# Kernel tuning notes

Measured on AMD Instinct MI355X. Metric: run time of the kernel, lower is better.

## Reference

```python
import jax, jax.numpy as jnp
import numpy as np

B, D, T = 4, 1024, 512      # z: [B, input_dim, T]
V, CD = 32000, 4096          # codebook: [codebook_size, codebook_dim]
EPS = 1e-12                  # F.normalize default eps


def setup_inputs() -> dict:
    key = jax.random.key(0)
    k1, k2, k3, k4 = jax.random.split(key, 4)
    z = jax.random.normal(k1, (B, D, T), dtype=jnp.float32)
    codebook = jax.random.normal(k2, (V, CD), dtype=jnp.float32) * 0.02
    cb_w = jax.random.normal(k3, (D, CD), dtype=jnp.float32) * 0.02  # torch Linear weight [out,in]
    cb_b = jax.random.normal(k4, (D,), dtype=jnp.float32) * 0.02
    return {"z": z, "codebook": codebook, "cb_w": cb_w, "cb_b": cb_b}


def _l2norm(x):
    n = jnp.sqrt(jnp.sum(x * x, axis=1, keepdims=True))
    return x / jnp.maximum(n, EPS)


def reference(z, codebook, cb_w, cb_b):
    # stride == 1, use_cblinear == True -> z_e = z
    z_e = z                                              # [B, D, T]
    proj_cb = codebook @ cb_w.T + cb_b                    # [V, D] cb_proj(codebook)

    # decode_latents
    enc = jnp.transpose(z_e, (0, 2, 1)).reshape(-1, D)    # (B*T, D)
    enc_n = _l2norm(enc)
    cb_n = _l2norm(proj_cb)
    dist = (jnp.sum(enc_n * enc_n, axis=1, keepdims=True)
            - 2.0 * enc_n @ cb_n.T
            + jnp.sum(cb_n * cb_n, axis=1)[None, :])      # (B*T, V)
    indices = jnp.argmax(-dist, axis=1).reshape(B, T)     # argmin distance
    z_q = jnp.transpose(proj_cb[indices], (0, 2, 1))      # gather un-normalized codes -> [B, D, T]

    commitment_loss = jnp.mean((z_e - jax.lax.stop_gradient(z_q)) ** 2, axis=(1, 2))  # [B]
    codebook_loss = jnp.mean((z_q - jax.lax.stop_gradient(z_e)) ** 2, axis=(1, 2))    # [B]
    z_q_st = z_e + jax.lax.stop_gradient(z_q - z_e)       # straight-through
    return z_q_st, indices, commitment_loss, codebook_loss
```

## Files before the change

### kernel.cpp

```cpp
#include <hip/hip_runtime.h>
#include <hip/hip_bf16.h>
#include <math.h>

#define B_  4
#define D_  1024
#define T_  512
#define V_  32000
#define CD_ 4096
#define NR  (B_*T_)
#define VT2 (V_/256)

typedef __attribute__((ext_vector_type(8))) short short8v;
typedef __attribute__((ext_vector_type(4))) float f32x4;

#define MFMA16(a,b,c) __builtin_amdgcn_mfma_f32_16x16x32_bf16((a),(b),(c),0,0,0)

#define ASM_VMCNT8() asm volatile("s_waitcnt vmcnt(8)" ::: "memory")
#define ASM_VMCNT0() asm volatile("s_waitcnt vmcnt(0)" ::: "memory")
#define ASM_LGKM0()  asm volatile("s_waitcnt lgkmcnt(0)" ::: "memory")
#define SCHED_BAR()  __builtin_amdgcn_sched_barrier(0)

__device__ __forceinline__ unsigned short f2bf(float f) {
    return __builtin_bit_cast(unsigned short, __float2bfloat16(f));
}
__device__ __forceinline__ float bf2f(unsigned short u) {
    unsigned int v = ((unsigned int)u) << 16;
    return __builtin_bit_cast(float, v);
}
__device__ __forceinline__ void glds16(const unsigned short* g, unsigned short* l) {
    __builtin_amdgcn_global_load_lds(
        (const __attribute__((address_space(1))) unsigned int*)g,
        (__attribute__((address_space(3))) unsigned int*)l, 16, 0, 0);
}
__device__ __forceinline__ void gldsf(const float* g, float* l) {
    __builtin_amdgcn_global_load_lds(
        (const __attribute__((address_space(1))) unsigned int*)g,
        (__attribute__((address_space(3))) unsigned int*)l, 16, 0, 0);
}
__device__ __forceinline__ void cvt8(const float4& x, const float4& y,
                                     short8v& h, short8v& l) {
    float xs[8] = {x.x, x.y, x.z, x.w, y.x, y.y, y.z, y.w};
    #pragma unroll
    for (int e = 0; e < 8; ++e) {
        unsigned short hb = f2bf(xs[e]);
        h[e] = (short)hb;
        l[e] = (short)f2bf(xs[e] - bf2f(hb));
    }
}
__device__ __forceinline__ int xcd_swz(int wg, int nwg) {
    int q = nwg >> 3, r = nwg & 7;
    int x = wg & 7, o = wg >> 3;
    return (x < r ? x * (q + 1) : r * (q + 1) + (x - r) * q) + o;
}

__global__ __launch_bounds__(256) void vq_cvt(const float* __restrict__ x,
                                              unsigned short* __restrict__ hi,
                                              unsigned short* __restrict__ lo,
                                              size_t n4) {
    size_t stride = (size_t)gridDim.x * 256;
    for (size_t i = (size_t)blockIdx.x * 256 + threadIdx.x; i < n4; i += stride) {
        float4 v = *(const float4*)(x + 4 * i);
        float xs[4] = {v.x, v.y, v.z, v.w};
        ushort4 h, l;
        unsigned short* hp = (unsigned short*)&h;
        unsigned short* lp = (unsigned short*)&l;
        #pragma unroll
        for (int e = 0; e < 4; ++e) {
            hp[e] = f2bf(xs[e]);
            lp[e] = f2bf(xs[e] - bf2f(hp[e]));
        }
        *(ushort4*)(hi + 4 * i) = h;
        *(ushort4*)(lo + 4 * i) = l;
    }
}

__global__ __launch_bounds__(512, 2) void vq_gemm1_f(
    const float* __restrict__ Acb,
    const unsigned short* __restrict__ Bhp, const unsigned short* __restrict__ Blp,
    const float* __restrict__ bias,
    unsigned short* __restrict__ Phi, unsigned short* __restrict__ Plo)
{
    __shared__ float          Af[2][8192];
    __shared__ unsigned short Bh[2][8192];
    __shared__ unsigned short Bl[2][8192];
    const int wg = xcd_swz(blockIdx.x, (V_/256) * (D_/256));
    const int mt = (wg >> 2) * 256;
    const int nt = (wg & 3) * 256;
    const int lane = threadIdx.x & 63, w = threadIdx.x >> 6;
    const int wr = w >> 2, wc = w & 3;
    const int r16 = lane & 15, kg = lane >> 4;
    const int lane8 = lane * 8, wr8 = wr * 8, wc4 = wc * 4;

    f32x4 acc[8][4];
    #pragma unroll
    for (int i = 0; i < 8; ++i)
        #pragma unroll
        for (int j = 0; j < 4; ++j) acc[i][j] = (f32x4){0.f, 0.f, 0.f, 0.f};

#define STAGE1F(b, kk) do {                                                   \
    if (w < 4) {                                                              \
        _Pragma("unroll")                                                     \
        for (int j = 0; j < 4; ++j) {                                         \
            const int sub = w * 4 + j;                                        \
            const float* g0 = Acb + (size_t)(mt + sub*16 + r16) * CD_         \
                              + (kk) + kg * 4;                                \
            gldsf(g0,      &Af[b][sub*512]);                                  \
            gldsf(g0 + 16, &Af[b][sub*512 + 256]);                            \
        }                                                                     \
    } else if (w < 6) {                                                       \
        const int sb = (w - 4) * 8;                                           \
        _Pragma("unroll")                                                     \
        for (int j = 0; j < 8; ++j)                                           \
            glds16(Bhp + (size_t)(nt + (sb+j)*16 + r16) * CD_ + (kk) + kg*8,  \
                   &Bh[b][(sb+j)*512]);                                       \
    } else {                                                                  \
        const int sb = (w - 6) * 8;                                           \
        _Pragma("unroll")                                                     \
        for (int j = 0; j < 8; ++j)                                           \
            glds16(Blp + (size_t)(nt + (sb+j)*16 + r16) * CD_ + (kk) + kg*8,  \
                   &Bl[b][(sb+j)*512]);                                       \
    }                                                                         \
} while (0)

    STAGE1F(0, 0);
    ASM_VMCNT0();
    __builtin_amdgcn_s_barrier();
    SCHED_BAR();

    const int NT = CD_ / 32;
    const int afrag = (kg >> 1) * 256 + (kg & 1) * 128 + r16 * 4;
    for (int t = 0; t < NT; ++t) {
        const int cur = t & 1;
        if (t + 1 < NT) {
            STAGE1F(cur ^ 1, (size_t)(t + 1) * 32);
            ASM_VMCNT8();
        } else {
            ASM_VMCNT0();
        }
        __builtin_amdgcn_s_barrier();
        SCHED_BAR();
        short8v bh[4], bl[4];
        #pragma unroll
        for (int nf = 0; nf < 4; ++nf) {
            bh[nf] = *(const short8v*)&Bh[cur][(wc4 + nf) * 512 + lane8];
            bl[nf] = *(const short8v*)&Bl[cur][(wc4 + nf) * 512 + lane8];
        }
        #pragma unroll
        for (int g = 0; g < 4; ++g) {
            const float* f0 = &Af[cur][(wr8 + 2*g) * 512 + afrag];
            const float* f1 = &Af[cur][(wr8 + 2*g + 1) * 512 + afrag];
            float4 x0 = *(const float4*)f0, x1 = *(const float4*)(f0 + 64);
            float4 y0 = *(const float4*)f1, y1 = *(const float4*)(f1 + 64);
            short8v a0h, a0l, a1h, a1l;
            cvt8(x0, x1, a0h, a0l);
            cvt8(y0, y1, a1h, a1l);
            __builtin_amdgcn_s_setprio(1);
            #pragma unroll
            for (int nf = 0; nf < 4; ++nf) {
                acc[2*g][nf]   = MFMA16(a0h, bh[nf], acc[2*g][nf]);
                acc[2*g][nf]   = MFMA16(a0h, bl[nf], acc[2*g][nf]);
                acc[2*g][nf]   = MFMA16(a0l, bh[nf], acc[2*g][nf]);
                acc[2*g+1][nf] = MFMA16(a1h, bh[nf], acc[2*g+1][nf]);
                acc[2*g+1][nf] = MFMA16(a1h, bl[nf], acc[2*g+1][nf]);
                acc[2*g+1][nf] = MFMA16(a1l, bh[nf], acc[2*g+1][nf]);
            }
            __builtin_amdgcn_s_setprio(0);
        }
        ASM_LGKM0();
        __builtin_amdgcn_s_barrier();
        SCHED_BAR();
    }
#undef STAGE1F

    #pragma unroll
    for (int nf = 0; nf < 4; ++nf) {
        const int col = nt + wc * 64 + nf * 16 + r16;
        const float bv = bias[col];
        #pragma unroll
        for (int mf = 0; mf < 8; ++mf) {
            const int rbase = mt + wr * 128 + mf * 16 + kg * 4;
            #pragma unroll
            for (int r = 0; r < 4; ++r) {
                float vv = acc[mf][nf][r] + bv;
                unsigned short h = f2bf(vv);
                unsigned short l = f2bf(vv - bf2f(h));
                size_t o = (size_t)(rbase + r) * D_ + col;
                Phi[o] = h; Plo[o] = l;
            }
        }
    }
}

#define T8_PHASE(pp, EXTRA)                                                   \
    {                                                                         \
        short8v aAh = *(const short8v*)&smem[cur][0][(wr8 + 2*(pp)) * 512 + lane8];     \
        short8v aAl = *(const short8v*)&smem[cur][1][(wr8 + 2*(pp)) * 512 + lane8];     \
        short8v aBh = *(const short8v*)&smem[cur][0][(wr8 + 2*(pp) + 1) * 512 + lane8]; \
        short8v aBl = *(const short8v*)&smem[cur][1][(wr8 + 2*(pp) + 1) * 512 + lane8]; \
        EXTRA;                                                                \
        SCHED_BAR();                                                          \
        __builtin_amdgcn_s_barrier();                                         \
        ASM_LGKM0();                                                          \
        SCHED_BAR();                                                          \
        __builtin_amdgcn_s_setprio(1);                                        \
        _Pragma("unroll")                                                     \
        for (int nf = 0; nf < 4; ++nf) {                                      \
            acc[2*(pp)][nf]   = MFMA16(aAh, bh[nf], acc[2*(pp)][nf]);         \
            acc[2*(pp)][nf]   = MFMA16(aAh, bl[nf], acc[2*(pp)][nf]);         \
            acc[2*(pp)][nf]   = MFMA16(aAl, bh[nf], acc[2*(pp)][nf]);         \
            acc[2*(pp)+1][nf] = MFMA16(aBh, bh[nf], acc[2*(pp)+1][nf]);       \
            acc[2*(pp)+1][nf] = MFMA16(aBh, bl[nf], acc[2*(pp)+1][nf]);       \
            acc[2*(pp)+1][nf] = MFMA16(aBl, bh[nf], acc[2*(pp)+1][nf]);       \
        }                                                                     \
        __builtin_amdgcn_s_setprio(0);                                        \
        __builtin_amdgcn_s_barrier();                                         \
        SCHED_BAR();                                                          \
    }

__global__ __launch_bounds__(512, 2) void vq_gemm2_t8(
    const unsigned short* __restrict__ Ahp, const unsigned short* __restrict__ Alp,
    const unsigned short* __restrict__ Bhp, const unsigned short* __restrict__ Blp,
    const float* __restrict__ ninv,
    float* __restrict__ pmax, int* __restrict__ pidx)
{
    __shared__ unsigned short smem[2][4][8192];
    const int wg = xcd_swz(blockIdx.x, (NR/256) * VT2);
    const int nid = wg >> 3;
    const int mt = (wg & 7) * 256;
    const int nt = nid * 256;

    f32x4 acc[8][4];
    #pragma unroll
    for (int i = 0; i < 8; ++i)
        #pragma unroll
        for (int j = 0; j < 4; ++j) acc[i][j] = (f32x4){0.f, 0.f, 0.f, 0.f};
    const int lane = threadIdx.x & 63, w = threadIdx.x >> 6;
    const int wr = w >> 2, wc = w & 3;
    const int r16 = lane & 15, kg = lane >> 4;
    const int lane8 = lane * 8, wr8 = wr * 8, wc4 = wc * 4;
    const int pw = w >> 1;
    const unsigned short* gplane = (pw == 0) ? Ahp : (pw == 1) ? Alp
                                   : (pw == 2) ? Bhp : Blp;
    const int baseRow = (pw < 2 ? mt : nt) + (w & 1) * 128 + r16;
    const unsigned short* gsrc = gplane + (size_t)baseRow * D_ + kg * 8;
    unsigned short* lb0 = &smem[0][pw][(w & 1) * 4096 + lane8];
    unsigned short* lb1 = &smem[1][pw][(w & 1) * 4096 + lane8];
    #pragma unroll
    for (int q = 0; q < 8; ++q)
        glds16(gsrc + (size_t)q * 16 * D_, lb0 + q * 512);
    ASM_VMCNT0();
    __builtin_amdgcn_s_barrier();
    SCHED_BAR();
    const int NT = D_ / 32;
    for (int t = 0; t < NT; ++t) {
        const int cur = t & 1;
        unsigned short* lbN = cur ? lb0 : lb1;
        short8v bh[4], bl[4];
        #pragma unroll
        for (int nf = 0; nf < 4; ++nf) {
            bh[nf] = *(const short8v*)&smem[cur][2][(wc4 + nf) * 512 + lane8];
            bl[nf] = *(const short8v*)&smem[cur][3][(wc4 + nf) * 512 + lane8];
        }
        T8_PHASE(0,
            if (t + 1 < NT) {
                const size_t kof = (size_t)(t + 1) * 32;
                _Pragma("unroll")
                for (int q = 0; q < 8; ++q)
                    glds16(gsrc + kof + (size_t)q * 16 * D_, lbN + q * 512);
            })
        T8_PHASE(1, (void)0)
        T8_PHASE(2, (void)0)
        T8_PHASE(3, if (t + 1 < NT) { ASM_VMCNT0(); })
    }

    float* redv = (float*)&smem[0][0][0];
    int*   redi = (int*)&smem[0][0][2048];
    float nv[4];
    #pragma unroll
    for (int nf = 0; nf < 4; ++nf) nv[nf] = ninv[nt + wc * 64 + nf * 16 + r16];
    #pragma unroll
    for (int mf = 0; mf < 8; ++mf) {
        #pragma unroll
        for (int r = 0; r < 4; ++r) {
            float best = -INFINITY; int bi = 0x7fffffff;
            #pragma unroll
            for (int nf = 0; nf < 4; ++nf) {
                float v = acc[mf][nf][r] * nv[nf];
                int ci = nt + wc * 64 + nf * 16 + r16;
                if (v > best || (v == best && ci < bi)) { best = v; bi = ci; }
            }
            #pragma unroll
            for (int m = 8; m >= 1; m >>= 1) {
                float ov = __shfl_xor(best, m, 16);
                int   oi = __shfl_xor(bi,   m, 16);
                if (ov > best || (ov == best && oi < bi)) { best = ov; bi = oi; }
            }
            if (r16 == 0) {
                int rl = wr * 128 + mf * 16 + kg * 4 + r;
                redv[rl * 4 + wc] = best; redi[rl * 4 + wc] = bi;
            }
        }
    }
    __builtin_amdgcn_s_barrier();
    if (threadIdx.x < 256) {
        float best = -INFINITY; int bi = 0x7fffffff;
        #pragma unroll
        for (int c = 0; c < 4; ++c) {
            float v = redv[threadIdx.x * 4 + c];
            int   i = redi[threadIdx.x * 4 + c];
            if (v > best || (v == best && i < bi)) { best = v; bi = i; }
        }
        size_t o = (size_t)(mt + threadIdx.x) * VT2 + nid;
        pmax[o] = best; pidx[o] = bi;
    }
}

__global__ __launch_bounds__(256) void vq_norms_pl(const unsigned short* __restrict__ ph,
                                                   const unsigned short* __restrict__ pl,
                                                   float* __restrict__ ninv) {
    const int row  = blockIdx.x * 4 + (threadIdx.x >> 6);
    const int lane = threadIdx.x & 63;
    float s = 0.f;
    #pragma unroll
    for (int q = 0; q < 2; ++q) {
        size_t o = (size_t)row * D_ + q * 512 + lane * 8;
        short8v h = *(const short8v*)(ph + o);
        short8v l = *(const short8v*)(pl + o);
        #pragma unroll
        for (int e = 0; e < 8; ++e) {
            float x = bf2f((unsigned short)h[e]) + bf2f((unsigned short)l[e]);
            s += x * x;
        }
    }
    #pragma unroll
    for (int off = 32; off >= 1; off >>= 1) s += __shfl_down(s, off);
    if (lane == 0) ninv[row] = 1.0f / fmaxf(sqrtf(s), 1e-12f);
}

__global__ __launch_bounds__(256) void vq_transpose_cvt(const float* __restrict__ z,
                                                        unsigned short* __restrict__ ehi,
                                                        unsigned short* __restrict__ elo) {
    __shared__ float tile[64][65];
    const int b = blockIdx.z, t0 = blockIdx.x * 64, d0 = blockIdx.y * 64;
    const int lane = threadIdx.x & 63, sub = threadIdx.x >> 6;
    for (int dd = sub; dd < 64; dd += 4)
        tile[dd][lane] = z[((size_t)b * D_ + d0 + dd) * T_ + t0 + lane];
    __syncthreads();
    for (int tt = sub; tt < 64; tt += 4) {
        float v = tile[lane][tt];
        unsigned short h = f2bf(v);
        unsigned short l = f2bf(v - bf2f(h));
        size_t o = (size_t)(b * T_ + t0 + tt) * D_ + d0 + lane;
        ehi[o] = h; elo[o] = l;
    }
}

__global__ __launch_bounds__(256) void vq_argmerge(const float* __restrict__ pmax,
                                                   const int* __restrict__ pidx,
                                                   int* __restrict__ idxw,
                                                   float* __restrict__ outI,
                                                   int vt) {
    const int i = blockIdx.x * 256 + threadIdx.x;
    if (i >= NR) return;
    float best = -INFINITY; int bi = 0;
    for (int c = 0; c < vt; c++) {
        float v = pmax[(size_t)i * vt + c];
        int   ii = pidx[(size_t)i * vt + c];
        if (v > best || (v == best && ii < bi)) { best = v; bi = ii; }
    }
    idxw[i] = bi;
    outI[i] = (float)bi;
}

__global__ __launch_bounds__(256) void vq_gather_pl(const unsigned short* __restrict__ ph,
                                                    const unsigned short* __restrict__ pl,
                                                    const int* __restrict__ idxw,
                                                    const float* __restrict__ z,
                                                    float* __restrict__ out0,
                                                    float* __restrict__ lpart) {
    __shared__ float zq[64][65];
    __shared__ int idx_s[64];
    __shared__ float wsum[4];
    const int b = blockIdx.z, t0 = blockIdx.x * 64, d0 = blockIdx.y * 64;
    const int tid = threadIdx.x;
    const int lane = tid & 63, sub = tid >> 6;
    if (tid < 64) idx_s[tid] = idxw[b * T_ + t0 + tid];
    __syncthreads();
    for (int tt = sub; tt < 64; tt += 4) {
        size_t o = (size_t)idx_s[tt] * D_ + d0 + lane;
        zq[tt][lane] = bf2f(ph[o]) + bf2f(pl[o]);
    }
    __syncthreads();
    float lacc = 0.f;
    for (int dd = sub; dd < 64; dd += 4) {
        const size_t base = ((size_t)b * D_ + d0 + dd) * T_ + t0 + lane;
        float q = zq[lane][dd];
        float zv = z[base];
        out0[base] = q;
        float dv = zv - q;
        lacc += dv * dv;
    }
    #pragma unroll
    for (int off = 32; off >= 1; off >>= 1) lacc += __shfl_down(lacc, off);
    if (lane == 0) wsum[sub] = lacc;
    __syncthreads();
    if (tid == 0)
        lpart[(blockIdx.z * 16 + blockIdx.y) * 8 + blockIdx.x] =
            wsum[0] + wsum[1] + wsum[2] + wsum[3];
}

__global__ void vq_loss(const float* __restrict__ lpart, float* __restrict__ outL) {
    const int b = threadIdx.x;
    if (b >= B_) return;
    float s = 0.f;
    for (int q = 0; q < 128; q++) s += lpart[b * 128 + q];
    s /= (float)(D_ * T_);
    outL[b]      = s;
    outL[B_ + b] = s;
}

extern "C" void kernel_launch(void* const* d_in, const int* in_sizes, int n_in,
                              void* d_out, int out_size, void* d_ws, size_t ws_size,
                              hipStream_t stream) {
    const float* z        = (const float*)d_in[0];
    const float* codebook = (const float*)d_in[1];
    const float* cb_w     = (const float*)d_in[2];
    const float* cb_b     = (const float*)d_in[3];

    float* out0 = (float*)d_out;
    float* outI = out0 + (size_t)B_*D_*T_;
    float* outL = outI + NR;

    char* p = (char*)d_ws;
    auto alloc = [&](size_t bytes) { char* r = p; p += (bytes + 255) & ~(size_t)255; return r; };
    unsigned short* w_hi = (unsigned short*)alloc((size_t)D_ * CD_ * 2);
    unsigned short* w_lo = (unsigned short*)alloc((size_t)D_ * CD_ * 2);
    unsigned short* p_hi = (unsigned short*)alloc((size_t)V_ * D_ * 2);
    unsigned short* p_lo = (unsigned short*)alloc((size_t)V_ * D_ * 2);
    unsigned short* e_hi = (unsigned short*)alloc((size_t)NR * D_ * 2);
    unsigned short* e_lo = (unsigned short*)alloc((size_t)NR * D_ * 2);
    float* ninv  = (float*)alloc((size_t)V_ * 4);
    float* pmax  = (float*)alloc((size_t)NR * VT2 * 4);
    int*   pidx  = (int*)  alloc((size_t)NR * VT2 * 4);
    int*   idxw  = (int*)  alloc((size_t)NR * 4);
    float* lpart = (float*)alloc((size_t)2048 * 4);

    vq_cvt<<<512, 256, 0, stream>>>(cb_w, w_hi, w_lo, (size_t)D_ * CD_ / 4);
    vq_transpose_cvt<<<dim3(T_/64, D_/64, B_), 256, 0, stream>>>(z, e_hi, e_lo);

    vq_gemm1_f<<<(V_/256) * (D_/256), 512, 0, stream>>>(codebook, w_hi, w_lo,
                                                        cb_b, p_hi, p_lo);
    vq_norms_pl<<<V_/4, 256, 0, stream>>>(p_hi, p_lo, ninv);
    vq_gemm2_t8<<<(NR/256) * VT2, 512, 0, stream>>>(e_hi, e_lo, p_hi, p_lo,
                                                    ninv, pmax, pidx);
    vq_argmerge<<<NR/256, 256, 0, stream>>>(pmax, pidx, idxw, outI, VT2);
    vq_gather_pl<<<dim3(T_/64, D_/64, B_), 256, 0, stream>>>(p_hi, p_lo, idxw, z,
                                                             out0, lpart);
    vq_loss<<<1, 64, 0, stream>>>(lpart, outL);
}
```

Baseline: 1.573 ms.

## Pre-split codebook into bf16 hi/lo planes and reuse pipelined t8 GEMM for projection

Adds a separate pass that converts the whole fp32 codebook into bf16 hi/lo planes. The projection GEMM then becomes a copy of the phased t8 kernel structure already used for the distance GEMM, with all warps issuing global-to-LDS loads and prefetches interleaved into the MFMA phases. This removes the in-loop fp32-to-bf16 split of A fragments, which was repeated for each of the four N tiles, and replaces the warp-specialized loader with the pipelined scheme. In exchange it writes and re-reads about 512 MB of extra bf16 planes and needs a larger workspace. The weight conversion kernel is also widened to 8 elements per thread.

Result: faster. 1.539 ms (median of 2 runs) (-2.2%).

```diff
diff --git a/kernel.cpp b/kernel.cpp
--- a/kernel.cpp
+++ b/kernel.cpp
@@ -9,6 +9,7 @@
 #define CD_ 4096
 #define NR  (B_*T_)
 #define VT2 (V_/256)
+#define NTILE1 ((V_/256)*(D_/256))
 
 typedef __attribute__((ext_vector_type(8))) short short8v;
 typedef __attribute__((ext_vector_type(4))) float f32x4;
@@ -32,11 +33,6 @@
         (const __attribute__((address_space(1))) unsigned int*)g,
         (__attribute__((address_space(3))) unsigned int*)l, 16, 0, 0);
 }
-__device__ __forceinline__ void gldsf(const float* g, float* l) {
-    __builtin_amdgcn_global_load_lds(
-        (const __attribute__((address_space(1))) unsigned int*)g,
-        (__attribute__((address_space(3))) unsigned int*)l, 16, 0, 0);
-}
 __device__ __forceinline__ void cvt8(const float4& x, const float4& y,
                                      short8v& h, short8v& l) {
     float xs[8] = {x.x, x.y, x.z, x.w, y.x, y.y, y.z, y.w};
@@ -53,141 +49,18 @@
     return (x < r ? x * (q + 1) : r * (q + 1) + (x - r) * q) + o;
 }
 
-__global__ __launch_bounds__(256) void vq_cvt(const float* __restrict__ x,
-                                              unsigned short* __restrict__ hi,
-                                              unsigned short* __restrict__ lo,
-                                              size_t n4) {
+__global__ __launch_bounds__(256) void vq_cvt8(const float* __restrict__ x,
+                                               unsigned short* __restrict__ hi,
+                                               unsigned short* __restrict__ lo,
+                                               size_t n8) {
     size_t stride = (size_t)gridDim.x * 256;
-    for (size_t i = (size_t)blockIdx.x * 256 + threadIdx.x; i < n4; i += stride) {
-        float4 v = *(const float4*)(x + 4 * i);
-        float xs[4] = {v.x, v.y, v.z, v.w};
-        ushort4 h, l;
-        unsigned short* hp = (unsigned short*)&h;
-        unsigned short* lp = (unsigned short*)&l;
-        #pragma unroll
-        for (int e = 0; e < 4; ++e) {
-            hp[e] = f2bf(xs[e]);
-            lp[e] = f2bf(xs[e] - bf2f(hp[e]));
-        }
-        *(ushort4*)(hi + 4 * i) = h;
-        *(ushort4*)(lo + 4 * i) = l;
-    }
-}
-
-__global__ __launch_bounds__(512, 2) void vq_gemm1_f(
-    const float* __restrict__ Acb,
-    const unsigned short* __restrict__ Bhp, const unsigned short* __restrict__ Blp,
-    const float* __restrict__ bias,
-    unsigned short* __restrict__ Phi, unsigned short* __restrict__ Plo)
-{
-    __shared__ float          Af[2][8192];
-    __shared__ unsigned short Bh[2][8192];
-    __shared__ unsigned short Bl[2][8192];
-    const int wg = xcd_swz(blockIdx.x, (V_/256) * (D_/256));
-    const int mt = (wg >> 2) * 256;
-    const int nt = (wg & 3) * 256;
-    const int lane = threadIdx.x & 63, w = threadIdx.x >> 6;
-    const int wr = w >> 2, wc = w & 3;
-    const int r16 = lane & 15, kg = lane >> 4;
-    const int lane8 = lane * 8, wr8 = wr * 8, wc4 = wc * 4;
-
-    f32x4 acc[8][4];
-    #pragma unroll
-    for (int i = 0; i < 8; ++i)
-        #pragma unroll
-        for (int j = 0; j < 4; ++j) acc[i][j] = (f32x4){0.f, 0.f, 0.f, 0.f};
-
-#define STAGE1F(b, kk) do {                                                   \
-    if (w < 4) {                                                              \
-        _Pragma("unroll")                                                     \
-        for (int j = 0; j < 4; ++j) {                                         \
-            const int sub = w * 4 + j;                                        \
-            const float* g0 = Acb + (size_t)(mt + sub*16 + r16) * CD_         \
-                              + (kk) + kg * 4;                                \
-            gldsf(g0,      &Af[b][sub*512]);                                  \
-            gldsf(g0 + 16, &Af[b][sub*512 + 256]);                            \
-        }                                                                     \
-    } else if (w < 6) {                                                       \
-        const int sb = (w - 4) * 8;                                           \
-        _Pragma("unroll")                                                     \
-        for (int j = 0; j < 8; ++j)                                           \
-            glds16(Bhp + (size_t)(nt + (sb+j)*16 + r16) * CD_ + (kk) + kg*8,  \
-                   &Bh[b][(sb+j)*512]);                                       \
-    } else {                                                                  \
-        const int sb = (w - 6) * 8;                                           \
-        _Pragma("unroll")                                                     \
-        for (int j = 0; j < 8; ++j)                                           \
-            glds16(Blp + (size_t)(nt + (sb+j)*16 + r16) * CD_ + (kk) + kg*8,  \
-                   &Bl[b][(sb+j)*512]);                                       \
-    }                                                                         \
-} while (0)
-
-    STAGE1F(0, 0);
-    ASM_VMCNT0();
-    __builtin_amdgcn_s_barrier();
-    SCHED_BAR();
-
-    const int NT = CD_ / 32;
-    const int afrag = (kg >> 1) * 256 + (kg & 1) * 128 + r16 * 4;
-    for (int t = 0; t < NT; ++t) {
-        const int cur = t & 1;
-        if (t + 1 < NT) {
-            STAGE1F(cur ^ 1, (size_t)(t + 1) * 32);
-            ASM_VMCNT8();
-        } else {
-            ASM_VMCNT0();
-        }
-        __builtin_amdgcn_s_barrier();
-        SCHED_BAR();
-        short8v bh[4], bl[4];
-        #pragma unroll
-        for (int nf = 0; nf < 4; ++nf) {
-            bh[nf] = *(const short8v*)&Bh[cur][(wc4 + nf) * 512 + lane8];
-            bl[nf] = *(const short8v*)&Bl[cur][(wc4 + nf) * 512 + lane8];
-        }
-        #pragma unroll
-        for (int g = 0; g < 4; ++g) {
-            const float* f0 = &Af[cur][(wr8 + 2*g) * 512 + afrag];
-            const float* f1 = &Af[cur][(wr8 + 2*g + 1) * 512 + afrag];
-            float4 x0 = *(const float4*)f0, x1 = *(const float4*)(f0 + 64);
-            float4 y0 = *(const float4*)f1, y1 = *(const float4*)(f1 + 64);
-            short8v a0h, a0l, a1h, a1l;
-            cvt8(x0, x1, a0h, a0l);
-            cvt8(y0, y1, a1h, a1l);
-            __builtin_amdgcn_s_setprio(1);
-            #pragma unroll
-            for (int nf = 0; nf < 4; ++nf) {
-                acc[2*g][nf]   = MFMA16(a0h, bh[nf], acc[2*g][nf]);
-                acc[2*g][nf]   = MFMA16(a0h, bl[nf], acc[2*g][nf]);
-                acc[2*g][nf]   = MFMA16(a0l, bh[nf], acc[2*g][nf]);
-                acc[2*g+1][nf] = MFMA16(a1h, bh[nf], acc[2*g+1][nf]);
-                acc[2*g+1][nf] = MFMA16(a1h, bl[nf], acc[2*g+1][nf]);
-                acc[2*g+1][nf] = MFMA16(a1l, bh[nf], acc[2*g+1][nf]);
-            }
-            __builtin_amdgcn_s_setprio(0);
-        }
-        ASM_LGKM0();
-        __builtin_amdgcn_s_barrier();
-        SCHED_BAR();
-    }
-#undef STAGE1F
-
-    #pragma unroll
-    for (int nf = 0; nf < 4; ++nf) {
-        const int col = nt + wc * 64 + nf * 16 + r16;
-        const float bv = bias[col];
-        #pragma unroll
-        for (int mf = 0; mf < 8; ++mf) {
-            const int rbase = mt + wr * 128 + mf * 16 + kg * 4;
-            #pragma unroll
-            for (int r = 0; r < 4; ++r) {
-                float vv = acc[mf][nf][r] + bv;
-                unsigned short h = f2bf(vv);
-                unsigned short l = f2bf(vv - bf2f(h));
-                size_t o = (size_t)(rbase + r) * D_ + col;
-                Phi[o] = h; Plo[o] = l;
-            }
-        }
+    for (size_t i = (size_t)blockIdx.x * 256 + threadIdx.x; i < n8; i += stride) {
+        float4 a = *(const float4*)(x + 8 * i);
+        float4 b = *(const float4*)(x + 8 * i + 4);
+        short8v h, l;
+        cvt8(a, b, h, l);
+        *(short8v*)(hi + 8 * i) = h;
+        *(short8v*)(lo + 8 * i) = l;
     }
 }
 
@@ -217,6 +90,81 @@
         SCHED_BAR();                                                          \
     }
 
+__global__ __launch_bounds__(512, 2) void vq_gemm1_t8(
+    const unsigned short* __restrict__ Ahp, const unsigned short* __restrict__ Alp,
+    const unsigned short* __restrict__ Bhp, const unsigned short* __restrict__ Blp,
+    const float* __restrict__ bias,
+    unsigned short* __restrict__ Phi, unsigned short* __restrict__ Plo)
+{
+    __shared__ unsigned short smem[2][4][8192];
+    const int wg = xcd_swz(blockIdx.x, NTILE1);
+    const int mt = (wg >> 2) * 256;
+    const int nt = (wg & 3) * 256;
+    const int lane = threadIdx.x & 63, w = threadIdx.x >> 6;
+    const int wr = w >> 2, wc = w & 3;
+    const int r16 = lane & 15, kg = lane >> 4;
+    const int lane8 = lane * 8, wr8 = wr * 8, wc4 = wc * 4;
+    const int pw = w >> 1;
+    const unsigned short* gplane = (pw == 0) ? Ahp : (pw == 1) ? Alp
+                                   : (pw == 2) ? Bhp : Blp;
+    const int baseRow = (pw < 2 ? mt : nt) + (w & 1) * 128 + r16;
+    const unsigned short* gsrc = gplane + (size_t)baseRow * CD_ + kg * 8;
+    unsigned short* lb0 = &smem[0][pw][(w & 1) * 4096 + lane8];
+    unsigned short* lb1 = &smem[1][pw][(w & 1) * 4096 + lane8];
+
+    f32x4 acc[8][4];
+    #pragma unroll
+    for (int i = 0; i < 8; ++i)
+        #pragma unroll
+        for (int j = 0; j < 4; ++j) acc[i][j] = (f32x4){0.f, 0.f, 0.f, 0.f};
+
+    #pragma unroll
+    for (int q = 0; q < 8; ++q)
+        glds16(gsrc + (size_t)q * 16 * CD_, lb0 + q * 512);
+    ASM_VMCNT0();
+    __builtin_amdgcn_s_barrier();
+    SCHED_BAR();
+    const int NT = CD_ / 32;
+    for (int t = 0; t < NT; ++t) {
+        const int cur = t & 1;
+        unsigned short* lbN = cur ? lb0 : lb1;
+        short8v bh[4], bl[4];
+        #pragma unroll
+        for (int nf = 0; nf < 4; ++nf) {
+            bh[nf] = *(const short8v*)&smem[cur][2][(wc4 + nf) * 512 + lane8];
+            bl[nf] = *(const short8v*)&smem[cur][3][(wc4 + nf) * 512 + lane8];
+        }
+        T8_PHASE(0,
+            if (t + 1 < NT) {
+                const size_t kof = (size_t)(t + 1) * 32;
+                _Pragma("unroll")
+                for (int q = 0; q < 8; ++q)
+                    glds16(gsrc + kof + (size_t)q * 16 * CD_, lbN + q * 512);
+            })
+        T8_PHASE(1, (void)0)
+        T8_PHASE(2, (void)0)
+        T8_PHASE(3, if (t + 1 < NT) { ASM_VMCNT0(); })
+    }
+
+    #pragma unroll
+    for (int nf = 0; nf < 4; ++nf) {
+        const int col = nt + wc * 64 + nf * 16 + r16;
+        const float bv = bias[col];
+        #pragma unroll
+        for (int mf = 0; mf < 8; ++mf) {
+            const int rbase = mt + wr * 128 + mf * 16 + kg * 4;
+            #pragma unroll
+            for (int r = 0; r < 4; ++r) {
+                float vv = acc[mf][nf][r] + bv;
+                unsigned short h = f2bf(vv);
+                unsigned short l = f2bf(vv - bf2f(h));
+                size_t o = (size_t)(rbase + r) * D_ + col;
+                Phi[o] = h; Plo[o] = l;
+            }
+        }
+    }
+}
+
 __global__ __launch_bounds__(512, 2) void vq_gemm2_t8(
     const unsigned short* __restrict__ Ahp, const unsigned short* __restrict__ Alp,
     const unsigned short* __restrict__ Bhp, const unsigned short* __restrict__ Blp,
@@ -444,12 +392,15 @@
     int*   pidx  = (int*)  alloc((size_t)NR * VT2 * 4);
     int*   idxw  = (int*)  alloc((size_t)NR * 4);
     float* lpart = (float*)alloc((size_t)2048 * 4);
-
-    vq_cvt<<<512, 256, 0, stream>>>(cb_w, w_hi, w_lo, (size_t)D_ * CD_ / 4);
+    unsigned short* c_hi = (unsigned short*)alloc((size_t)V_ * CD_ * 2);
+    unsigned short* c_lo = (unsigned short*)alloc((size_t)V_ * CD_ * 2);
+
+    vq_cvt8<<<512, 256, 0, stream>>>(cb_w, w_hi, w_lo, (size_t)D_ * CD_ / 8);
     vq_transpose_cvt<<<dim3(T_/64, D_/64, B_), 256, 0, stream>>>(z, e_hi, e_lo);
-
-    vq_gemm1_f<<<(V_/256) * (D_/256), 512, 0, stream>>>(codebook, w_hi, w_lo,
-                                                        cb_b, p_hi, p_lo);
+    vq_cvt8<<<2048, 256, 0, stream>>>(codebook, c_hi, c_lo, (size_t)V_ * CD_ / 8);
+
+    vq_gemm1_t8<<<NTILE1, 512, 0, stream>>>(c_hi, c_lo, w_hi, w_lo,
+                                            cb_b, p_hi, p_lo);
     vq_norms_pl<<<V_/4, 256, 0, stream>>>(p_hi, p_lo, ninv);
     vq_gemm2_t8<<<(NR/256) * VT2, 512, 0, stream>>>(e_hi, e_lo, p_hi, p_lo,
                                                     ninv, pmax, pidx);
```
